# Performance work log

Measured on AMD Instinct MI355X. Metric: run time of the kernel, lower is better.

Reference implementation:

```python
import jax, jax.numpy as jnp
import numpy as np

WIN = 1024
HOP = 256

def setup_inputs() -> dict:
    key = jax.random.key(0)
    x = jax.random.normal(key, (16, WIN, 2048), dtype=jnp.float32)
    return {"x": x}

def reference(x) -> jnp.ndarray:
    # Overlap-add: y[b, f*hop + c] += x[b, c, f]
    B, win, n_frames = x.shape
    hop = HOP
    out_len = (n_frames - 1) * hop + win
    idx = jnp.arange(win)[:, None] + hop * jnp.arange(n_frames)[None, :]
    y = jnp.zeros((B, out_len), dtype=x.dtype)
    y = y.at[:, idx].add(x)
    return y
```

## Files before the change

### kernel.cpp

```cpp
#include <hip/hip_runtime.h>


constexpr int BATCH   = 16;
constexpr int WIN     = 1024;
constexpr int HOP     = 256;
constexpr int NF      = 2048;
constexpr int OUT_LEN = (NF - 1) * HOP + WIN;
constexpr int GTOT    = OUT_LEN / HOP;
constexpr int FT      = 128;
constexpr int NTILES  = (GTOT + FT - 1) / FT;
constexpr int RB      = 32;
constexpr int NRS     = HOP / RB;

typedef float f4a __attribute__((ext_vector_type(4), aligned(16)));

__global__ __launch_bounds__(256, 2)
void oadd_kernel(const float* __restrict__ x, float* __restrict__ y) {
    __shared__ float L[4][RB][FT];

    const int tid   = threadIdx.x;
    const int tile  = blockIdx.x;
    const int rsp   = blockIdx.y;
    const int b     = blockIdx.z;
    const int g0    = tile * FT;
    const int rbase = rsp * RB;

    const int lane = tid & 63;
    const int w    = tid >> 6;
    const int fq   = (lane & 31) * 4;
    const int rh   = lane >> 5;

    const float* __restrict__ xb = x + (size_t)b * WIN * NF;

    const bool interior = (g0 >= 3) && (g0 + FT <= NF);

    if (interior) {
        #pragma unroll
        for (int it = 0; it < 4; ++it) {
            const int rl = it * 8 + w * 2;
            #pragma unroll
            for (int k = 0; k < 4; ++k) {
                const float* src = xb + (size_t)(k * HOP + rbase + rl + rh) * NF
                                      + (g0 + fq - k);
                __builtin_amdgcn_global_load_lds(
                    (const __attribute__((address_space(1))) unsigned int*)src,
                    (__attribute__((address_space(3))) unsigned int*)&L[k][rl][0],
                    16, 0, 0);
            }
        }
    } else {
        #pragma unroll
        for (int it = 0; it < 4; ++it) {
            const int rl = it * 8 + w * 2 + rh;
            #pragma unroll
            for (int k = 0; k < 4; ++k) {
                const float* rp = xb + (size_t)(k * HOP + rbase + rl) * NF;
                #pragma unroll
                for (int m = 0; m < 4; ++m) {
                    const int f = g0 + fq + m - k;
                    L[k][rl][fq + m] = (f >= 0 && f < NF) ? rp[f] : 0.f;
                }
            }
        }
    }

    __syncthreads();

    float* __restrict__ yb = y + (size_t)b * OUT_LEN;
    const int jj = tid & 31;
    const int rq = tid >> 5;
    #pragma unroll
    for (int p = 0; p < 4; ++p) {
        const int j = p * 32 + jj;
        const int g = g0 + j;
        if (g < GTOT) {
            f4a v;
            #pragma unroll
            for (int m = 0; m < 4; ++m) {
                const int rl = rq * 4 + m;
                v[m] = (L[0][rl][j] + L[1][rl][j]) + (L[2][rl][j] + L[3][rl][j]);
            }
            *reinterpret_cast<f4a*>(&yb[(size_t)g * HOP + rbase + rq * 4]) = v;
        }
    }
}

extern "C" void kernel_launch(void* const* d_in, const int* in_sizes, int n_in,
                              void* d_out, int out_size, void* d_ws, size_t ws_size,
                              hipStream_t stream) {
    const float* x = (const float*)d_in[0];
    float* y = (float*)d_out;
    dim3 grid(NTILES, NRS, BATCH);
    oadd_kernel<<<grid, 256, 0, stream>>>(x, y);
}
```

Before: 40.89 us.

## Process two half-size tiles per block with split waits to overlap load and store

Halves the frame tile width and assigns two work items to each block, staging both into separate LDS buffers. Both direct-to-LDS loads are issued up front, and the wait uses partial vmcnt so the first item's reduction and store can proceed while the second item's loads are still in flight. The grid becomes 1D with manual index decoding. This adds hand-written waitcnt and barrier logic whose correctness depends on the exact load counts, and it doubles LDS per block.

```diff
diff --git a/kernel.cpp b/kernel.cpp
--- a/kernel.cpp
+++ b/kernel.cpp
@@ -7,82 +7,102 @@
 constexpr int NF      = 2048;
 constexpr int OUT_LEN = (NF - 1) * HOP + WIN;
 constexpr int GTOT    = OUT_LEN / HOP;
-constexpr int FT      = 128;
-constexpr int NTILES  = (GTOT + FT - 1) / FT;
+constexpr int FT      = 64;
+constexpr int NTILE   = (GTOT + FT - 1) / FT;
 constexpr int RB      = 32;
 constexpr int NRS     = HOP / RB;
+constexpr int NITEMS  = NTILE * NRS * BATCH;
+constexpr int NBLK    = NITEMS / 2;
 
 typedef float f4a __attribute__((ext_vector_type(4), aligned(16)));
 
 __global__ __launch_bounds__(256, 2)
 void oadd_kernel(const float* __restrict__ x, float* __restrict__ y) {
-    __shared__ float L[4][RB][FT];
+    __shared__ float L[2][4][RB][FT];
 
-    const int tid   = threadIdx.x;
-    const int tile  = blockIdx.x;
-    const int rsp   = blockIdx.y;
-    const int b     = blockIdx.z;
-    const int g0    = tile * FT;
-    const int rbase = rsp * RB;
-
+    const int tid  = threadIdx.x;
     const int lane = tid & 63;
     const int w    = tid >> 6;
-    const int fq   = (lane & 31) * 4;
-    const int rh   = lane >> 5;
+    const int fq   = (lane & 15) * 4;
+    const int sr   = lane >> 4;
 
-    const float* __restrict__ xb = x + (size_t)b * WIN * NF;
+    const int it0 = blockIdx.x * 2;
+    const int it1 = it0 + 1;
+    const int tA = it0 % NTILE, rA = (it0 / NTILE) & 7, bA = it0 / (NTILE * 8);
+    const int tB = it1 % NTILE, rB = (it1 / NTILE) & 7, bB = it1 / (NTILE * 8);
+    const int g0A = tA * FT, rbaseA = rA * RB;
+    const int g0B = tB * FT, rbaseB = rB * RB;
+    const float* __restrict__ xbA = x + (size_t)bA * WIN * NF;
+    const float* __restrict__ xbB = x + (size_t)bB * WIN * NF;
+    float* __restrict__ ybA = y + (size_t)bA * OUT_LEN;
+    float* __restrict__ ybB = y + (size_t)bB * OUT_LEN;
+    const bool intA = (g0A >= 3) && (g0A + FT <= NF);
+    const bool intB = (g0B >= 3) && (g0B + FT <= NF);
 
-    const bool interior = (g0 >= 3) && (g0 + FT <= NF);
-
-    if (interior) {
+    auto fillDMA = [&](int s, int g0, int rbase, const float* __restrict__ xb) {
         #pragma unroll
-        for (int it = 0; it < 4; ++it) {
-            const int rl = it * 8 + w * 2;
+        for (int i = 0; i < 8; ++i) {
+            const int p   = w * 8 + i;
+            const int k   = p >> 3;
+            const int rl0 = (p & 7) * 4;
+            const float* src = xb + (size_t)(k * HOP + rbase + rl0 + sr) * NF
+                                  + (g0 + fq - k);
+            __builtin_amdgcn_global_load_lds(
+                (const __attribute__((address_space(1))) unsigned int*)src,
+                (__attribute__((address_space(3))) unsigned int*)&L[s][k][rl0][0],
+                16, 0, 0);
+        }
+    };
+    auto fillGuard = [&](int s, int g0, int rbase, const float* __restrict__ xb) {
+        #pragma unroll
+        for (int i = 0; i < 8; ++i) {
+            const int p  = w * 8 + i;
+            const int k  = p >> 3;
+            const int rl = (p & 7) * 4 + sr;
+            const float* rp = xb + (size_t)(k * HOP + rbase + rl) * NF;
             #pragma unroll
-            for (int k = 0; k < 4; ++k) {
-                const float* src = xb + (size_t)(k * HOP + rbase + rl + rh) * NF
-                                      + (g0 + fq - k);
-                __builtin_amdgcn_global_load_lds(
-                    (const __attribute__((address_space(1))) unsigned int*)src,
-                    (__attribute__((address_space(3))) unsigned int*)&L[k][rl][0],
-                    16, 0, 0);
+            for (int m = 0; m < 4; ++m) {
+                const int f = g0 + fq + m - k;
+                L[s][k][rl][fq + m] = (f >= 0 && f < NF) ? rp[f] : 0.f;
             }
         }
-    } else {
+        asm volatile("s_waitcnt lgkmcnt(0)" ::: "memory");
+    };
+    auto phase2 = [&](int s, int g0, int rbase, float* __restrict__ yb) {
+        const int jj = tid & 31;
+        const int rq = tid >> 5;
         #pragma unroll
-        for (int it = 0; it < 4; ++it) {
-            const int rl = it * 8 + w * 2 + rh;
-            #pragma unroll
-            for (int k = 0; k < 4; ++k) {
-                const float* rp = xb + (size_t)(k * HOP + rbase + rl) * NF;
+        for (int p = 0; p < 2; ++p) {
+            const int j = p * 32 + jj;
+            const int g = g0 + j;
+            if (g < GTOT) {
+                f4a v;
                 #pragma unroll
                 for (int m = 0; m < 4; ++m) {
-                    const int f = g0 + fq + m - k;
-                    L[k][rl][fq + m] = (f >= 0 && f < NF) ? rp[f] : 0.f;
+                    const int rl = rq * 4 + m;
+                    v[m] = (L[s][0][rl][j] + L[s][1][rl][j])
+                         + (L[s][2][rl][j] + L[s][3][rl][j]);
                 }
+                *reinterpret_cast<f4a*>(&yb[(size_t)g * HOP + rbase + rq * 4]) = v;
             }
         }
-    }
+    };
 
-    __syncthreads();
+    if (intA) fillDMA(0, g0A, rbaseA, xbA); else fillGuard(0, g0A, rbaseA, xbA);
+    if (intB) fillDMA(1, g0B, rbaseB, xbB); else fillGuard(1, g0B, rbaseB, xbB);
 
-    float* __restrict__ yb = y + (size_t)b * OUT_LEN;
-    const int jj = tid & 31;
-    const int rq = tid >> 5;
-    #pragma unroll
-    for (int p = 0; p < 4; ++p) {
-        const int j = p * 32 + jj;
-        const int g = g0 + j;
-        if (g < GTOT) {
-            f4a v;
-            #pragma unroll
-            for (int m = 0; m < 4; ++m) {
-                const int rl = rq * 4 + m;
-                v[m] = (L[0][rl][j] + L[1][rl][j]) + (L[2][rl][j] + L[3][rl][j]);
-            }
-            *reinterpret_cast<f4a*>(&yb[(size_t)g * HOP + rbase + rq * 4]) = v;
-        }
-    }
+    if (intB) { asm volatile("s_waitcnt vmcnt(8)" ::: "memory"); }
+    else      { asm volatile("s_waitcnt vmcnt(0)" ::: "memory"); }
+    __builtin_amdgcn_s_barrier();
+    __builtin_amdgcn_sched_barrier(0);
+
+    phase2(0, g0A, rbaseA, ybA);
+
+    asm volatile("s_waitcnt vmcnt(0)" ::: "memory");
+    __builtin_amdgcn_s_barrier();
+    __builtin_amdgcn_sched_barrier(0);
+
+    phase2(1, g0B, rbaseB, ybB);
 }
 
 extern "C" void kernel_launch(void* const* d_in, const int* in_sizes, int n_in,
@@ -90,6 +110,5 @@
                               hipStream_t stream) {
     const float* x = (const float*)d_in[0];
     float* y = (float*)d_out;
-    dim3 grid(NTILES, NRS, BATCH);
-    oadd_kernel<<<grid, 256, 0, stream>>>(x, y);
+    oadd_kernel<<<dim3(NBLK), 256, 0, stream>>>(x, y);
 }
```

Result: no change. 40.70 us (-0.5%).

## Convert overlap-add kernel to persistent blocks with multi-buffered async LDS prefetch

Applied to the files above, without the earlier changes.

Replaces the one-tile-per-block grid with 512 persistent blocks that loop over smaller tiles (64 frames × 16 rows). Global-to-LDS loads for upcoming tiles are issued two iterations ahead into a 4-slot ring, with explicit vmcnt waits, so loads overlap with the reduction and stores. Edge tiles now load through the async path too, and out-of-range contributions are masked when the sums are formed instead of loading zeros. This aims to hide memory latency and cut launch and tail overhead. In exchange it adds index-decode work per tile and relies on hand-counted waitcnt and barrier ordering.

```diff
diff --git a/kernel.cpp b/kernel.cpp
--- a/kernel.cpp
+++ b/kernel.cpp
@@ -7,81 +7,108 @@
 constexpr int NF      = 2048;
 constexpr int OUT_LEN = (NF - 1) * HOP + WIN;
 constexpr int GTOT    = OUT_LEN / HOP;
-constexpr int FT      = 128;
-constexpr int NTILES  = (GTOT + FT - 1) / FT;
-constexpr int RB      = 32;
+constexpr int FT      = 64;
+constexpr int NTILE   = (GTOT + FT - 1) / FT;
+constexpr int RB      = 16;
 constexpr int NRS     = HOP / RB;
+constexpr int NITEMS  = NTILE * NRS * BATCH;
+constexpr int NBLK    = 512;
+constexpr int NBUF    = 4;
 
 typedef float f4a __attribute__((ext_vector_type(4), aligned(16)));
 
 __global__ __launch_bounds__(256, 2)
 void oadd_kernel(const float* __restrict__ x, float* __restrict__ y) {
-    __shared__ float L[4][RB][FT];
+    __shared__ float L[NBUF][4][RB][FT];
 
-    const int tid   = threadIdx.x;
-    const int tile  = blockIdx.x;
-    const int rsp   = blockIdx.y;
-    const int b     = blockIdx.z;
-    const int g0    = tile * FT;
-    const int rbase = rsp * RB;
+    const int tid = threadIdx.x;
+    const int w   = tid >> 6;
+    const int l   = tid & 63;
+    const int sr  = l >> 4;
+    const int c4  = (l & 15) * 4;
 
-    const int lane = tid & 63;
-    const int w    = tid >> 6;
-    const int fq   = (lane & 31) * 4;
-    const int rh   = lane >> 5;
+    const int j   = tid & 63;
+    const int rq  = tid >> 6;
 
-    const float* __restrict__ xb = x + (size_t)b * WIN * NF;
+    const int rem = NITEMS - (NITEMS / NBLK) * NBLK;
+    const int T   = (int)blockIdx.x < rem ? NITEMS / NBLK + 1 : NITEMS / NBLK;
 
-    const bool interior = (g0 >= 3) && (g0 + FT <= NF);
+    auto decode = [&](int t, int& g0, int& rbase, int& b, int& mode) {
+        const unsigned it   = blockIdx.x + (unsigned)t * NBLK;
+        const unsigned tile = it % NTILE;
+        const unsigned rest = it / NTILE;
+        const unsigned rsp  = rest % NRS;
+        b     = rest / NRS;
+        g0    = tile * FT;
+        rbase = rsp * RB;
+        mode  = (tile == 0) ? 1 : ((tile == NTILE - 1) ? 2 : 0);
+    };
 
-    if (interior) {
+    auto fill = [&](int t, int s) {
+        int g0, rbase, b, mode; decode(t, g0, rbase, b, mode);
+        const int fcol = (mode == 2) ? (NF - FT) + c4 : g0 + c4 - w;
+        const float* src0 = x + (size_t)b * WIN * NF
+                              + (size_t)(w * HOP + rbase + sr) * NF + fcol;
         #pragma unroll
-        for (int it = 0; it < 4; ++it) {
-            const int rl = it * 8 + w * 2;
-            #pragma unroll
-            for (int k = 0; k < 4; ++k) {
-                const float* src = xb + (size_t)(k * HOP + rbase + rl + rh) * NF
-                                      + (g0 + fq - k);
-                __builtin_amdgcn_global_load_lds(
-                    (const __attribute__((address_space(1))) unsigned int*)src,
-                    (__attribute__((address_space(3))) unsigned int*)&L[k][rl][0],
-                    16, 0, 0);
-            }
+        for (int i = 0; i < 4; ++i) {
+            __builtin_amdgcn_global_load_lds(
+                (const __attribute__((address_space(1))) unsigned int*)(src0 + (size_t)(4 * i) * NF),
+                (__attribute__((address_space(3))) unsigned int*)&L[s][w][4 * i][0],
+                16, 0, 0);
         }
-    } else {
-        #pragma unroll
-        for (int it = 0; it < 4; ++it) {
-            const int rl = it * 8 + w * 2 + rh;
-            #pragma unroll
-            for (int k = 0; k < 4; ++k) {
-                const float* rp = xb + (size_t)(k * HOP + rbase + rl) * NF;
-                #pragma unroll
-                for (int m = 0; m < 4; ++m) {
-                    const int f = g0 + fq + m - k;
-                    L[k][rl][fq + m] = (f >= 0 && f < NF) ? rp[f] : 0.f;
-                }
-            }
-        }
-    }
+    };
 
-    __syncthreads();
-
-    float* __restrict__ yb = y + (size_t)b * OUT_LEN;
-    const int jj = tid & 31;
-    const int rq = tid >> 5;
-    #pragma unroll
-    for (int p = 0; p < 4; ++p) {
-        const int j = p * 32 + jj;
-        const int g = g0 + j;
-        if (g < GTOT) {
+    auto phase2 = [&](int t, int s) {
+        int g0, rbase, b, mode; decode(t, g0, rbase, b, mode);
+        float* __restrict__ yb = y + (size_t)b * OUT_LEN;
+        if (mode == 0) {
             f4a v;
             #pragma unroll
             for (int m = 0; m < 4; ++m) {
                 const int rl = rq * 4 + m;
-                v[m] = (L[0][rl][j] + L[1][rl][j]) + (L[2][rl][j] + L[3][rl][j]);
+                v[m] = (L[s][0][rl][j] + L[s][1][rl][j])
+                     + (L[s][2][rl][j] + L[s][3][rl][j]);
             }
-            *reinterpret_cast<f4a*>(&yb[(size_t)g * HOP + rbase + rq * 4]) = v;
+            *reinterpret_cast<f4a*>(&yb[(size_t)(g0 + j) * HOP + rbase + rq * 4]) = v;
+        } else if (mode == 1) {
+            f4a v;
+            #pragma unroll
+            for (int m = 0; m < 4; ++m) {
+                const int rl = rq * 4 + m;
+                float a = L[s][0][rl][j];
+                a += (j >= 1) ? L[s][1][rl][j] : 0.f;
+                a += (j >= 2) ? L[s][2][rl][j] : 0.f;
+                a += (j >= 3) ? L[s][3][rl][j] : 0.f;
+                v[m] = a;
+            }
+            *reinterpret_cast<f4a*>(&yb[(size_t)(g0 + j) * HOP + rbase + rq * 4]) = v;
+        } else {
+            if (g0 + j < GTOT) {
+                f4a v;
+                #pragma unroll
+                for (int m = 0; m < 4; ++m) {
+                    const int rl = rq * 4 + m;
+                    float a = 0.f;
+                    #pragma unroll
+                    for (int k = 1; k < 4; ++k)
+                        a += (k > j) ? L[s][k][rl][FT - k + j] : 0.f;
+                    v[m] = a;
+                }
+                *reinterpret_cast<f4a*>(&yb[(size_t)(g0 + j) * HOP + rbase + rq * 4]) = v;
+            }
         }
+    };
+
+    fill(0, 0);
+    if (T > 1) fill(1, 1);
+
+    for (int t = 0; t < T; ++t) {
+        if (t + 2 < T) fill(t + 2, (t + 2) & 3);
+        if (t + 2 < T)      asm volatile("s_waitcnt vmcnt(8)" ::: "memory");
+        else if (t + 1 < T) asm volatile("s_waitcnt vmcnt(4)" ::: "memory");
+        else                asm volatile("s_waitcnt vmcnt(0)" ::: "memory");
+        asm volatile("s_barrier" ::: "memory");
+        phase2(t, t & 3);
     }
 }
 
@@ -90,6 +117,5 @@
                               hipStream_t stream) {
     const float* x = (const float*)d_in[0];
     float* y = (float*)d_out;
-    dim3 grid(NTILES, NRS, BATCH);
-    oadd_kernel<<<grid, 256, 0, stream>>>(x, y);
+    oadd_kernel<<<dim3(NBLK), 256, 0, stream>>>(x, y);
 }
```

Result: faster. 37.14 us (-9.2%).

## Make each wave own a row strip and double-buffer tiles via async LDS loads

Applied to the files above, without the earlier changes.

Replaces the one-block-per-tile grid with a persistent-style layout: each wavefront owns a 4-row strip for one batch and walks 8 or 9 frame tiles. Each tile is double-buffered in LDS, with the next tile's global_load_lds issued before summing the current one and hand-written s_waitcnt vmcnt counts setting the overlap. Block-level __syncthreads is removed because each wave uses only its own LDS slice, and edge tiles are handled with special-case index logic. This aims to hide load latency and cut launch and sync overhead, at the cost of fewer blocks (512) and fragile hand-tuned waitcnt values.

```diff
diff --git a/kernel.cpp b/kernel.cpp
--- a/kernel.cpp
+++ b/kernel.cpp
@@ -8,80 +8,105 @@
 constexpr int OUT_LEN = (NF - 1) * HOP + WIN;
 constexpr int GTOT    = OUT_LEN / HOP;
 constexpr int FT      = 128;
-constexpr int NTILES  = (GTOT + FT - 1) / FT;
-constexpr int RB      = 32;
-constexpr int NRS     = HOP / RB;
+constexpr int RBW     = 4;
+constexpr int NBLK    = 512;
 
 typedef float f4a __attribute__((ext_vector_type(4), aligned(16)));
 
 __global__ __launch_bounds__(256, 2)
 void oadd_kernel(const float* __restrict__ x, float* __restrict__ y) {
-    __shared__ float L[4][RB][FT];
+    __shared__ float L[4][2][4][RBW][FT];
 
-    const int tid   = threadIdx.x;
-    const int tile  = blockIdx.x;
-    const int rsp   = blockIdx.y;
-    const int b     = blockIdx.z;
-    const int g0    = tile * FT;
-    const int rbase = rsp * RB;
+    const int tid = threadIdx.x;
+    const int w   = tid >> 6;
+    const int l   = tid & 63;
 
-    const int lane = tid & 63;
-    const int w    = tid >> 6;
-    const int fq   = (lane & 31) * 4;
-    const int rh   = lane >> 5;
+    const int wid = blockIdx.x * 4 + w;
+    const int b   = wid >> 7;
+    const int rsp = (wid >> 1) & 63;
+    const int tg  = wid & 1;
+    const int T   = tg ? 9 : 8;
+    const int rbase = rsp * RBW;
 
     const float* __restrict__ xb = x + (size_t)b * WIN * NF;
+    float* __restrict__ yb = y + (size_t)b * OUT_LEN;
 
-    const bool interior = (g0 >= 3) && (g0 + FT <= NF);
+    const int ch = (l & 31) * 4;
+    const int rh = l >> 5;
 
-    if (interior) {
+    auto fill = [&](int t, int s) {
+        const int tile = tg * 8 + t;
+        const bool m2  = (tile == 16);
+        const int g0   = tile * FT;
         #pragma unroll
-        for (int it = 0; it < 4; ++it) {
-            const int rl = it * 8 + w * 2;
+        for (int k = 0; k < 4; ++k) {
+            const int col = m2 ? (NF - FT) + ch : g0 + ch - k;
             #pragma unroll
-            for (int k = 0; k < 4; ++k) {
-                const float* src = xb + (size_t)(k * HOP + rbase + rl + rh) * NF
-                                      + (g0 + fq - k);
+            for (int i = 0; i < 2; ++i) {
+                const int row = k * HOP + rbase + i * 2 + rh;
+                const float* src = xb + (size_t)row * NF + col;
                 __builtin_amdgcn_global_load_lds(
                     (const __attribute__((address_space(1))) unsigned int*)src,
-                    (__attribute__((address_space(3))) unsigned int*)&L[k][rl][0],
+                    (__attribute__((address_space(3))) unsigned int*)&L[w][s][k][i * 2][0],
                     16, 0, 0);
             }
         }
-    } else {
-        #pragma unroll
-        for (int it = 0; it < 4; ++it) {
-            const int rl = it * 8 + w * 2 + rh;
+    };
+
+    auto phase2 = [&](int t, int s) {
+        const int tile = tg * 8 + t;
+        const int g0   = tile * FT;
+        if (tile == 0) {
             #pragma unroll
-            for (int k = 0; k < 4; ++k) {
-                const float* rp = xb + (size_t)(k * HOP + rbase + rl) * NF;
+            for (int p = 0; p < 2; ++p) {
+                const int j = p * 64 + l;
+                f4a v;
                 #pragma unroll
                 for (int m = 0; m < 4; ++m) {
-                    const int f = g0 + fq + m - k;
-                    L[k][rl][fq + m] = (f >= 0 && f < NF) ? rp[f] : 0.f;
+                    float a = L[w][s][0][m][j];
+                    if (j >= 1) a += L[w][s][1][m][j];
+                    if (j >= 2) a += L[w][s][2][m][j];
+                    if (j >= 3) a += L[w][s][3][m][j];
+                    v[m] = a;
                 }
+                *reinterpret_cast<f4a*>(&yb[(size_t)(g0 + j) * HOP + rbase]) = v;
+            }
+        } else if (tile == 16) {
+            if (l < 3) {
+                const int j = l;
+                f4a v;
+                #pragma unroll
+                for (int m = 0; m < 4; ++m) {
+                    float a = 0.f;
+                    #pragma unroll
+                    for (int k = 1; k < 4; ++k)
+                        if (k > j) a += L[w][s][k][m][FT - k + j];
+                    v[m] = a;
+                }
+                *reinterpret_cast<f4a*>(&yb[(size_t)(g0 + j) * HOP + rbase]) = v;
+            }
+        } else {
+            #pragma unroll
+            for (int p = 0; p < 2; ++p) {
+                const int j = p * 64 + l;
+                f4a v;
+                #pragma unroll
+                for (int m = 0; m < 4; ++m) {
+                    v[m] = (L[w][s][0][m][j] + L[w][s][1][m][j])
+                         + (L[w][s][2][m][j] + L[w][s][3][m][j]);
+                }
+                *reinterpret_cast<f4a*>(&yb[(size_t)(g0 + j) * HOP + rbase]) = v;
             }
         }
-    }
+    };
 
-    __syncthreads();
-
-    float* __restrict__ yb = y + (size_t)b * OUT_LEN;
-    const int jj = tid & 31;
-    const int rq = tid >> 5;
-    #pragma unroll
-    for (int p = 0; p < 4; ++p) {
-        const int j = p * 32 + jj;
-        const int g = g0 + j;
-        if (g < GTOT) {
-            f4a v;
-            #pragma unroll
-            for (int m = 0; m < 4; ++m) {
-                const int rl = rq * 4 + m;
-                v[m] = (L[0][rl][j] + L[1][rl][j]) + (L[2][rl][j] + L[3][rl][j]);
-            }
-            *reinterpret_cast<f4a*>(&yb[(size_t)g * HOP + rbase + rq * 4]) = v;
-        }
+    fill(0, 0);
+    for (int t = 0; t < T; ++t) {
+        if (t + 1 < T) fill(t + 1, (t + 1) & 1);
+        if (t == 0)         asm volatile("s_waitcnt vmcnt(8)"  ::: "memory");
+        else if (t + 1 < T) asm volatile("s_waitcnt vmcnt(10)" ::: "memory");
+        else                asm volatile("s_waitcnt vmcnt(2)"  ::: "memory");
+        phase2(t, t & 1);
     }
 }
 
@@ -90,6 +115,5 @@
                               hipStream_t stream) {
     const float* x = (const float*)d_in[0];
     float* y = (float*)d_out;
-    dim3 grid(NTILES, NRS, BATCH);
-    oadd_kernel<<<grid, 256, 0, stream>>>(x, y);
+    oadd_kernel<<<dim3(NBLK), 256, 0, stream>>>(x, y);
 }
```

After: 41.54 us. About the same (+1.6%).
